# Performance work log

Measured on AMD Instinct MI355X. Metric: run time of the kernel, lower is better.

Reference implementation:

```python
import jax, jax.numpy as jnp
import numpy as np

N_EMBED = 256
N_HEADS = 4
HEAD_SIZE = N_EMBED // N_HEADS  # 64
BLOCK_SIZE = 768
LN_EPS = 1e-5


def layer_norm(x, g, b):
    mu = jnp.mean(x, axis=-1, keepdims=True)
    var = jnp.var(x, axis=-1, keepdims=True)
    return (x - mu) * jax.lax.rsqrt(var + LN_EPS) * g + b


def setup_inputs() -> dict:
    key = jax.random.key(0)
    ks = jax.random.split(key, 12)
    B, T, C, H, hs = 32, BLOCK_SIZE, N_EMBED, N_HEADS, HEAD_SIZE
    s_in = 1.0 / np.sqrt(C)
    s_ff = 1.0 / np.sqrt(4 * C)
    return {
        "x": jax.random.normal(ks[0], (B, T, C), jnp.float32),
        # per-head projections, stacked: [H, C, hs]
        "Wq": jax.random.normal(ks[1], (H, C, hs), jnp.float32) * s_in,
        "Wk": jax.random.normal(ks[2], (H, C, hs), jnp.float32) * s_in,
        "Wv": jax.random.normal(ks[3], (H, C, hs), jnp.float32) * s_in,
        "Wo": jax.random.normal(ks[4], (C, C), jnp.float32) * s_in,
        "bo": jnp.zeros((C,), jnp.float32),
        "W1": jax.random.normal(ks[5], (C, 4 * C), jnp.float32) * s_in,
        "b1": jnp.zeros((4 * C,), jnp.float32),
        "W2": jax.random.normal(ks[6], (4 * C, C), jnp.float32) * s_ff,
        "b2": jnp.zeros((C,), jnp.float32),
        "g1": jnp.ones((C,), jnp.float32),
        "be1": jnp.zeros((C,), jnp.float32),
        "g2": jnp.ones((C,), jnp.float32),
        "be2": jnp.zeros((C,), jnp.float32),
    }


def reference(x, Wq, Wk, Wv, Wo, bo, W1, b1, W2, b2, g1, be1, g2, be2):
    B, T, C = x.shape
    # --- multi-head causal self-attention (pre-LN) ---
    h = layer_norm(x, g1, be1)
    q = jnp.einsum("btc,hcd->bhtd", h, Wq)
    k = jnp.einsum("btc,hcd->bhtd", h, Wk)
    v = jnp.einsum("btc,hcd->bhtd", h, Wv)
    scores = jnp.einsum("bhtd,bhsd->bhts", q, k) * (HEAD_SIZE ** -0.5)
    causal = jnp.tril(jnp.ones((T, T), bool))
    scores = jnp.where(causal, scores, -jnp.inf)
    attn = jax.nn.softmax(scores, axis=-1)  # dropout = identity (eval)
    o = jnp.einsum("bhts,bhsd->bhtd", attn, v)
    o = o.transpose(0, 2, 1, 3).reshape(B, T, C)  # concat heads
    x = x + o @ Wo + bo
    # --- feed-forward (pre-LN) ---
    h2 = layer_norm(x, g2, be2)
    x = x + jax.nn.relu(h2 @ W1 + b1) @ W2 + b2
    return x
```

## Files before the change

### kernel.cpp

```cpp
#include <hip/hip_runtime.h>
#include <stdint.h>

using short8   = __attribute__((ext_vector_type(8))) short;
using f32x4    = __attribute__((ext_vector_type(4))) float;
using ushort4v = __attribute__((ext_vector_type(4))) unsigned short;
using uint2v   = __attribute__((ext_vector_type(2))) unsigned int;

#define CSC  0.1803368801111f
#define FIXC 20.0f

__device__ __forceinline__ unsigned short f2bf(float f) {
    unsigned int u = __builtin_bit_cast(unsigned int, f);
    u += 0x7FFFu + ((u >> 16) & 1u);
    return (unsigned short)(u >> 16);
}
__device__ __forceinline__ float bf2f(unsigned short s) {
    unsigned int u = ((unsigned int)s) << 16;
    return __builtin_bit_cast(float, u);
}
__device__ __forceinline__ unsigned pk2bf(float a, float b) {
    unsigned r;
    asm("v_cvt_pk_bf16_f32 %0, %1, %2" : "=v"(r) : "v"(a), "v"(b));
    return r;
}

__device__ __forceinline__ void gload16(const void* g, void* l) {
    __builtin_amdgcn_global_load_lds(
        (const __attribute__((address_space(1))) void*)(uintptr_t)g,
        (__attribute__((address_space(3))) void*)(unsigned)(uintptr_t)l,
        16, 0, 0);
}

__device__ __forceinline__ uint2v ln_row_pk(f32x4 v, f32x4 gv, f32x4 bvv) {
    float s  = v[0] + v[1] + v[2] + v[3];
    float s2 = v[0]*v[0] + v[1]*v[1] + v[2]*v[2] + v[3]*v[3];
    for (int m = 1; m < 64; m <<= 1) {
        s  += __shfl_xor(s,  m, 64);
        s2 += __shfl_xor(s2, m, 64);
    }
    float mu  = s * (1.0f / 256.0f);
    float var = s2 * (1.0f / 256.0f) - mu * mu;
    float rs  = rsqrtf(var + 1e-5f);
    float r0 = (v[0] - mu) * rs * gv[0] + bvv[0];
    float r1 = (v[1] - mu) * rs * gv[1] + bvv[1];
    float r2 = (v[2] - mu) * rs * gv[2] + bvv[2];
    float r3 = (v[3] - mu) * rs * gv[3] + bvv[3];
    uint2v u; u[0] = pk2bf(r0, r1); u[1] = pk2bf(r2, r3);
    return u;
}

__global__ __launch_bounds__(256) void prep_k(const float* __restrict__ x, const float* __restrict__ g1,
                                              const float* __restrict__ be1, unsigned short* __restrict__ h,
                                              const float* __restrict__ Wq, const float* __restrict__ Wk,
                                              const float* __restrict__ Wv, const float* __restrict__ Wo,
                                              const float* __restrict__ W1, const float* __restrict__ W2,
                                              unsigned short* __restrict__ wpackT, unsigned short* __restrict__ woT,
                                              unsigned short* __restrict__ w1T, unsigned short* __restrict__ w2T) {
    __shared__ float t[64][65];
    if (blockIdx.x >= 192) {
        int row  = (blockIdx.x - 192) * 4 + (threadIdx.x >> 6);
        int lane = threadIdx.x & 63;
        f32x4 v = *(const f32x4*)(x + (size_t)row * 256 + lane * 4);
        f32x4 gv = *(const f32x4*)(g1 + lane * 4);
        f32x4 bv = *(const f32x4*)(be1 + lane * 4);
        uint2v u = ln_row_pk(v, gv, bv);
        *(uint2v*)(h + (size_t)row * 256 + lane * 4) = u;
        return;
    }
    const int bid = blockIdx.x;
    const float* in; unsigned short* out;
    int R, C, r0, c0;
    if (bid < 48) {
        int z = bid >> 2, cx = bid & 3;
        int qkv = z >> 2, hh = z & 3;
        in = ((qkv == 0) ? Wq : (qkv == 1) ? Wk : Wv) + (size_t)hh * 256 * 64;
        out = wpackT + (size_t)(qkv * 256 + hh * 64) * 256;
        R = 256; C = 64; r0 = cx * 64; c0 = 0;
    } else if (bid < 64) {
        int tt = bid - 48;
        in = Wo; out = woT; R = 256; C = 256; r0 = (tt >> 2) * 64; c0 = (tt & 3) * 64;
    } else if (bid < 128) {
        int tt = bid - 64;
        in = W1; out = w1T; R = 256; C = 1024; r0 = (tt & 3) * 64; c0 = (tt >> 2) * 64;
    } else {
        int tt = bid - 128;
        in = W2; out = w2T; R = 1024; C = 256; r0 = (tt & 15) * 64; c0 = (tt >> 4) * 64;
    }
    const int tx = threadIdx.x & 63, ty = threadIdx.x >> 6;
    #pragma unroll
    for (int i = 0; i < 64; i += 4)
        t[i + ty][tx] = in[(size_t)(r0 + i + ty) * C + c0 + tx];
    __syncthreads();
    #pragma unroll
    for (int i = 0; i < 64; i += 4)
        out[(size_t)(c0 + i + ty) * R + r0 + tx] = f2bf(t[tx][i + ty]);
}

__global__ __launch_bounds__(256) void qkv_k(const unsigned short* __restrict__ h,
                                             const unsigned short* __restrict__ wpackT,
                                             unsigned short* __restrict__ qk,
                                             unsigned short* __restrict__ vT) {
    __shared__ unsigned short As[128 * 64];
    __shared__ unsigned short Bs[128 * 64];
    const int tid  = threadIdx.x;
    const int lane = tid & 63;
    const int w    = tid >> 6;
    const int wm   = w >> 1, wn = w & 1;
    const int l15  = lane & 15, l4 = lane >> 4;
    const int bid  = blockIdx.x;

    const unsigned short *A, *BT;
    unsigned short* outp;
    int bm, bn, N;
    float qsc = 1.0f;
    if (bid < 768) {
        const int xcd = bid & 7, i = bid >> 3;
        bm = xcd * 24 + (i >> 2);
        bn = i & 3;
        A = h; BT = wpackT; outp = qk; N = 512;
        if (bn < 2) qsc = CSC;
    } else {
        const int t = bid - 768;
        const int xcd = t & 7, j = t >> 3;
        bn = xcd * 24 + (j >> 1);
        bm = j & 1;
        A = wpackT + 512 * 256; BT = h; outp = vT; N = 24576;
    }
    const int K = 256;

    f32x4 acc[4][4] = {};

    const size_t K2 = (size_t)K * 2;
    const int i0   = w * 4096 + lane * 16;
    const int row0 = i0 >> 7;
    const int cb0  = (i0 & 127) ^ ((row0 & 7) << 4);
    const char* aSrc = (const char*)A  + ((size_t)(bm * 128 + row0)) * K2 + cb0;
    const char* bSrc = (const char*)BT + ((size_t)(bn * 128 + row0)) * K2 + cb0;

    for (int t = 0; t < 4; ++t) {
        {
            const char* aS = aSrc + (size_t)t * 128;
            const char* bS = bSrc + (size_t)t * 128;
            char* aD = (char*)&As[0] + w * 4096;
            char* bD = (char*)&Bs[0] + w * 4096;
            #pragma unroll
            for (int c = 0; c < 4; ++c) {
                gload16(aS + (size_t)c * 8 * K2, aD + c * 1024);
                gload16(bS + (size_t)c * 8 * K2, bD + c * 1024);
            }
        }
        __syncthreads();
        #pragma unroll
        for (int kf = 0; kf < 2; ++kf) {
            int kb = kf * 64 + l4 * 16;
            short8 af[4], bfr[4];
            #pragma unroll
            for (int mf = 0; mf < 4; ++mf) {
                int row = wm * 64 + mf * 16 + l15;
                af[mf] = *(const short8*)((const char*)&As[0] + ((row * 128 + kb) ^ ((row & 7) << 4)));
            }
            #pragma unroll
            for (int nf = 0; nf < 4; ++nf) {
                int row = wn * 64 + nf * 16 + l15;
                bfr[nf] = *(const short8*)((const char*)&Bs[0] + ((row * 128 + kb) ^ ((row & 7) << 4)));
            }
            #pragma unroll
            for (int mf = 0; mf < 4; ++mf)
                #pragma unroll
                for (int nf = 0; nf < 4; ++nf)
                    acc[mf][nf] = __builtin_amdgcn_mfma_f32_16x16x32_bf16(af[mf], bfr[nf], acc[mf][nf], 0, 0, 0);
        }
        __syncthreads();
    }

    #pragma unroll
    for (int nf = 0; nf < 4; ++nf) {
        int col = bn * 128 + wn * 64 + nf * 16 + l15;
        #pragma unroll
        for (int mf = 0; mf < 4; ++mf) {
            int row0o = bm * 128 + wm * 64 + mf * 16 + l4 * 4;
            size_t off = (size_t)row0o * N + col;
            unsigned p01 = pk2bf(acc[mf][nf][0] * qsc, acc[mf][nf][1] * qsc);
            unsigned p23 = pk2bf(acc[mf][nf][2] * qsc, acc[mf][nf][3] * qsc);
            outp[off]                 = (unsigned short)p01;
            outp[off + (size_t)N]     = (unsigned short)(p01 >> 16);
            outp[off + (size_t)N * 2] = (unsigned short)p23;
            outp[off + (size_t)N * 3] = (unsigned short)(p23 >> 16);
        }
    }
}

template <int EPI, bool DB>
__global__ __launch_bounds__(256) void gemm_bt(const unsigned short* __restrict__ A,
                                               const unsigned short* __restrict__ BT,
                                               void* __restrict__ outp,
                                               const float* __restrict__ bias,
                                               const void* __restrict__ resid,
                                               int K, int N) {
    __shared__ unsigned short As[DB ? 2 : 1][128 * 64];
    __shared__ unsigned short Bs[DB ? 2 : 1][128 * 64];
    const int tid  = threadIdx.x;
    const int lane = tid & 63;
    const int w    = tid >> 6;
    const int wm   = w >> 1, wn = w & 1;
    const int bm   = blockIdx.y, bn = blockIdx.x;
    const int l15  = lane & 15, l4 = lane >> 4;

    f32x4 acc[4][4] = {};

    const size_t K2 = (size_t)K * 2;
    const int i0   = w * 4096 + lane * 16;
    const int row0 = i0 >> 7;
    const int cb0  = (i0 & 127) ^ ((row0 & 7) << 4);
    const char* aSrc = (const char*)A  + ((size_t)(bm * 128 + row0)) * K2 + cb0;
    const char* bSrc = (const char*)BT + ((size_t)(bn * 128 + row0)) * K2 + cb0;
    const int nt = K >> 6;

    auto stage = [&](int t, int buf) {
        const char* aS = aSrc + (size_t)t * 128;
        const char* bS = bSrc + (size_t)t * 128;
        char* aD = (char*)&As[buf][0] + w * 4096;
        char* bD = (char*)&Bs[buf][0] + w * 4096;
        #pragma unroll
        for (int c = 0; c < 4; ++c) {
            gload16(aS + (size_t)c * 8 * K2, aD + c * 1024);
            gload16(bS + (size_t)c * 8 * K2, bD + c * 1024);
        }
    };
    auto compute = [&](int buf) {
        const char* AsB = (const char*)&As[buf][0];
        const char* BsB = (const char*)&Bs[buf][0];
        #pragma unroll
        for (int kf = 0; kf < 2; ++kf) {
            int kb = kf * 64 + l4 * 16;
            short8 af[4], bfr[4];
            #pragma unroll
            for (int mf = 0; mf < 4; ++mf) {
                int row = wm * 64 + mf * 16 + l15;
                af[mf] = *(const short8*)(AsB + ((row * 128 + kb) ^ ((row & 7) << 4)));
            }
            #pragma unroll
            for (int nf = 0; nf < 4; ++nf) {
                int row = wn * 64 + nf * 16 + l15;
                bfr[nf] = *(const short8*)(BsB + ((row * 128 + kb) ^ ((row & 7) << 4)));
            }
            #pragma unroll
            for (int mf = 0; mf < 4; ++mf)
                #pragma unroll
                for (int nf = 0; nf < 4; ++nf)
                    acc[mf][nf] = __builtin_amdgcn_mfma_f32_16x16x32_bf16(af[mf], bfr[nf], acc[mf][nf], 0, 0, 0);
        }
    };

    if (DB) {
        stage(0, 0);
        for (int t = 0; t < nt; ++t) {
            const int cur = t & 1;
            __syncthreads();
            if (t + 1 < nt) stage(t + 1, cur ^ 1);
            compute(cur);
        }
    } else {
        for (int t = 0; t < nt; ++t) {
            stage(t, 0);
            __syncthreads();
            compute(0);
            __syncthreads();
        }
    }

    #pragma unroll
    for (int nf = 0; nf < 4; ++nf) {
        int col = bn * 128 + wn * 64 + nf * 16 + l15;
        float bv = bias[col];
        #pragma unroll
        for (int mf = 0; mf < 4; ++mf) {
            int row0o = bm * 128 + wm * 64 + mf * 16 + l4 * 4;
            size_t off = (size_t)row0o * N + col;
            float v[4];
            #pragma unroll
            for (int r = 0; r < 4; ++r)
                v[r] = acc[mf][nf][r] + bv + ((const float*)resid)[off + (size_t)r * N];
            unsigned short* O = (unsigned short*)outp;
            unsigned p01 = pk2bf(v[0], v[1]), p23 = pk2bf(v[2], v[3]);
            O[off]                 = (unsigned short)p01;
            O[off + (size_t)N]     = (unsigned short)(p01 >> 16);
            O[off + (size_t)N * 2] = (unsigned short)p23;
            O[off + (size_t)N * 3] = (unsigned short)(p23 >> 16);
        }
    }
}

__global__ __launch_bounds__(256) void ff_fused(const unsigned short* __restrict__ x1b,
                                                const float* __restrict__ g2,
                                                const float* __restrict__ be2,
                                                const unsigned short* __restrict__ w1T,
                                                const unsigned short* __restrict__ w2T,
                                                const float* __restrict__ b1,
                                                const float* __restrict__ b2,
                                                float* __restrict__ out) {
    __shared__ unsigned short sA[4][64 * 64];
    __shared__ unsigned short sW[16384];
    __shared__ unsigned short sAct[64 * 64];
    const int tid = threadIdx.x, lane = tid & 63, w = tid >> 6;
    const int l15 = lane & 15, l4 = lane >> 4;
    const int wm = w >> 1, wn = w & 1;
    const int r0 = blockIdx.x * 64;

    {
        f32x4 gv = *(const f32x4*)(g2 + lane * 4);
        f32x4 bv = *(const f32x4*)(be2 + lane * 4);
        const int ks = lane >> 4, colb = (lane & 15) * 8;
        #pragma unroll
        for (int it = 0; it < 16; ++it) {
            int row = it * 4 + w;
            ushort4v u4 = *(const ushort4v*)(x1b + (size_t)(r0 + row) * 256 + lane * 4);
            f32x4 v;
            #pragma unroll
            for (int i = 0; i < 4; ++i) v[i] = bf2f(u4[i]);
            uint2v u = ln_row_pk(v, gv, bv);
            *(uint2v*)((char*)&sA[0][0] + ks * 8192 + row * 128 + (colb ^ ((row & 7) << 4))) = u;
        }
    }

    f32x4 oacc[2][8] = {};

    for (int c = 0; c < 16; ++c) {
        {
            const char* wb = (const char*)w1T + (size_t)(c * 64) * 512;
            #pragma unroll
            for (int g = 0; g < 8; ++g) {
                int j = g * 4096 + tid * 16;
                int ks = j >> 13, row = (j >> 7) & 63, cb = j & 127;
                gload16(wb + (size_t)row * 512 + ks * 128 + (cb ^ ((row & 7) << 4)),
                        (char*)&sW[0] + j);
            }
        }
        __syncthreads();

        f32x4 aacc[2][2] = {};
        __builtin_amdgcn_s_setprio(1);
        #pragma unroll
        for (int ks = 0; ks < 4; ++ks) {
            #pragma unroll
            for (int kf = 0; kf < 2; ++kf) {
                const int kb = kf * 64 + l4 * 16;
                short8 hf[2], wf[2];
                #pragma unroll
                for (int mf = 0; mf < 2; ++mf) {
                    int row = wm * 32 + mf * 16 + l15;
                    hf[mf] = *(const short8*)((const char*)&sA[ks][0] + ((row * 128 + kb) ^ ((row & 7) << 4)));
                }
                #pragma unroll
                for (int nf = 0; nf < 2; ++nf) {
                    int row = wn * 32 + nf * 16 + l15;
                    wf[nf] = *(const short8*)((const char*)&sW[ks * 4096] + ((row * 128 + kb) ^ ((row & 7) << 4)));
                }
                #pragma unroll
                for (int mf = 0; mf < 2; ++mf)
                    #pragma unroll
                    for (int nf = 0; nf < 2; ++nf)
                        aacc[mf][nf] = __builtin_amdgcn_mfma_f32_16x16x32_bf16(wf[nf], hf[mf], aacc[mf][nf], 0, 0, 0);
            }
        }
        __builtin_amdgcn_s_setprio(0);
        #pragma unroll
        for (int mf = 0; mf < 2; ++mf)
            #pragma unroll
            for (int nf = 0; nf < 2; ++nf) {
                int nl = wn * 32 + nf * 16 + l4 * 4;
                f32x4 bv = *(const f32x4*)(b1 + c * 64 + nl);
                float v0 = aacc[mf][nf][0] + bv[0]; v0 = v0 > 0.0f ? v0 : 0.0f;
                float v1 = aacc[mf][nf][1] + bv[1]; v1 = v1 > 0.0f ? v1 : 0.0f;
                float v2 = aacc[mf][nf][2] + bv[2]; v2 = v2 > 0.0f ? v2 : 0.0f;
                float v3 = aacc[mf][nf][3] + bv[3]; v3 = v3 > 0.0f ? v3 : 0.0f;
                uint2v u; u[0] = pk2bf(v0, v1); u[1] = pk2bf(v2, v3);
                int m = wm * 32 + mf * 16 + l15;
                *(uint2v*)((char*)&sAct[0] + ((m * 128 + nl * 2) ^ ((m & 7) << 4))) = u;
            }
        __syncthreads();

        {
            const char* wb = (const char*)w2T + (size_t)c * 128;
            #pragma unroll
            for (int g = 0; g < 8; ++g) {
                int j = g * 4096 + tid * 16;
                int row = j >> 7, cb = j & 127;
                gload16(wb + (size_t)row * 2048 + (cb ^ ((row & 7) << 4)),
                        (char*)&sW[0] + j);
            }
        }
        __syncthreads();

        __builtin_amdgcn_s_setprio(1);
        #pragma unroll
        for (int kf = 0; kf < 2; ++kf) {
            const int kb = kf * 64 + l4 * 16;
            short8 af[2], wf[8];
            #pragma unroll
            for (int mf = 0; mf < 2; ++mf) {
                int row = wm * 32 + mf * 16 + l15;
                af[mf] = *(const short8*)((const char*)&sAct[0] + ((row * 128 + kb) ^ ((row & 7) << 4)));
            }
            #pragma unroll
            for (int nf = 0; nf < 8; ++nf) {
                int row = wn * 128 + nf * 16 + l15;
                wf[nf] = *(const short8*)((const char*)&sW[0] + ((row * 128 + kb) ^ ((row & 7) << 4)));
            }
            #pragma unroll
            for (int mf = 0; mf < 2; ++mf)
                #pragma unroll
                for (int nf = 0; nf < 8; ++nf)
                    oacc[mf][nf] = __builtin_amdgcn_mfma_f32_16x16x32_bf16(af[mf], wf[nf], oacc[mf][nf], 0, 0, 0);
        }
        __builtin_amdgcn_s_setprio(0);
        __syncthreads();
    }

    #pragma unroll
    for (int nf = 0; nf < 8; ++nf) {
        const int col = wn * 128 + nf * 16 + l15;
        const float bv = b2[col];
        #pragma unroll
        for (int mf = 0; mf < 2; ++mf) {
            const int row = r0 + wm * 32 + mf * 16 + l4 * 4;
            const size_t off = (size_t)row * 256 + col;
            #pragma unroll
            for (int r = 0; r < 4; ++r)
                out[off + (size_t)r * 256] = oacc[mf][nf][r] + bv + bf2f(x1b[off + (size_t)r * 256]);
        }
    }
}

__global__ __launch_bounds__(256) void attn_k(const unsigned short* __restrict__ qk,
                                              const unsigned short* __restrict__ vT,
                                              unsigned short* __restrict__ o) {
    __shared__ unsigned short Ks[2][64 * 64];
    __shared__ unsigned short Vt[2][64 * 64];
    __shared__ unsigned short Pl[4][16 * 64];
    const int tid = threadIdx.x, lane = tid & 63, w = tid >> 6;
    const int l15 = lane & 15, l4 = lane >> 4;
    const int gid = blockIdx.x;
    const int xcd = gid & 7, slot = gid >> 3;
    const int sl6 = slot / 6;
    const int bh  = xcd * 16 + sl6;
    const int x   = slot - sl6 * 6;
    const int qb1 = x, qb2 = 11 - x;
    const int b = bh >> 2, h = bh & 3;
    const unsigned short* Qb = qk + (size_t)b * 768 * 512 + h * 64;
    const char* Kg = (const char*)(Qb + 256);
    const char* Vg = (const char*)(vT + (size_t)(h * 64) * 24576 + (size_t)b * 768);
    const int t01 = qb1 * 64, t02 = qb2 * 64;
    const int tq1 = t01 + w * 16 + l15;
    const int tq2 = t02 + w * 16 + l15;

    short8 q1f0 = *(const short8*)(Qb + (size_t)tq1 * 512 + l4 * 8);
    short8 q1f1 = *(const short8*)(Qb + (size_t)tq1 * 512 + 32 + l4 * 8);
    short8 q2f0 = *(const short8*)(Qb + (size_t)tq2 * 512 + l4 * 8);
    short8 q2f1 = *(const short8*)(Qb + (size_t)tq2 * 512 + 32 + l4 * 8);

    const int srow = w * 16 + (lane >> 3);
    const int scb  = ((lane & 7) * 16) ^ ((srow & 7) << 4);
    const char* kSrc = Kg + (size_t)srow * 1024 + scb;
    const char* vSrc = Vg + (size_t)srow * 49152 + scb;
    char* kDst0 = (char*)&Ks[0][0] + w * 2048;
    char* vDst0 = (char*)&Vt[0][0] + w * 2048;

    f32x4 oA[4] = {}, oB[4] = {};
    float lsA = 0.0f, lsB = 0.0f;
    unsigned short* Pw = &Pl[w][0];
    const char* KsB;
    const char* VtB;
    int sb = 0;

    auto do_tile = [&](short8 qf0, short8 qf1, f32x4 (&oacc)[4], float& lsum, bool diag, int tq) {
        f32x4 sacc[4] = {};
        __builtin_amdgcn_s_setprio(1);
        #pragma unroll
        for (int kf = 0; kf < 2; ++kf) {
            const int kb = kf * 64 + l4 * 16;
            short8 qf = kf ? qf1 : qf0;
            #pragma unroll
            for (int nf = 0; nf < 4; ++nf) {
                int sr = nf * 16 + l15;
                short8 kfr = *(const short8*)(KsB + ((sr * 128 + kb) ^ ((sr & 7) << 4)));
                sacc[nf] = __builtin_amdgcn_mfma_f32_16x16x32_bf16(kfr, qf, sacc[nf], 0, 0, 0);
            }
        }
        __builtin_amdgcn_s_setprio(0);

        if (diag) {
            #pragma unroll
            for (int nf = 0; nf < 4; ++nf)
                #pragma unroll
                for (int r = 0; r < 4; ++r) {
                    int s = sb * 64 + nf * 16 + l4 * 4 + r;
                    if (s > tq) sacc[nf][r] = -1e30f;
                }
        }
        float psum = 0.0f;
        #pragma unroll
        for (int nf = 0; nf < 4; ++nf) {
            float p0 = __builtin_amdgcn_exp2f(sacc[nf][0] - FIXC);
            float p1 = __builtin_amdgcn_exp2f(sacc[nf][1] - FIXC);
            float p2 = __builtin_amdgcn_exp2f(sacc[nf][2] - FIXC);
            float p3 = __builtin_amdgcn_exp2f(sacc[nf][3] - FIXC);
            psum += (p0 + p1) + (p2 + p3);
            uint2v u; u[0] = pk2bf(p0, p1); u[1] = pk2bf(p2, p3);
            *(uint2v*)((char*)Pw + ((l15 * 128 + nf * 32 + l4 * 8) ^ ((l15 & 7) << 4))) = u;
        }
        psum += __shfl_xor(psum, 16, 64);
        psum += __shfl_xor(psum, 32, 64);
        lsum += psum;

        __builtin_amdgcn_s_setprio(1);
        #pragma unroll
        for (int kf = 0; kf < 2; ++kf) {
            const int kb = kf * 64 + l4 * 16;
            short8 pa = *(const short8*)((const char*)Pw + ((l15 * 128 + kb) ^ ((l15 & 7) << 4)));
            #pragma unroll
            for (int nf = 0; nf < 4; ++nf) {
                int dr = nf * 16 + l15;
                short8 vfr = *(const short8*)(VtB + ((dr * 128 + kb) ^ ((dr & 7) << 4)));
                oacc[nf] = __builtin_amdgcn_mfma_f32_16x16x32_bf16(pa, vfr, oacc[nf], 0, 0, 0);
            }
        }
        __builtin_amdgcn_s_setprio(0);
    };

    gload16(kSrc, kDst0);                 gload16(kSrc + 8 * 1024, kDst0 + 1024);
    gload16(vSrc, vDst0);                 gload16(vSrc + 8 * 49152, vDst0 + 1024);

    for (sb = 0; sb <= qb2; ++sb) {
        const int pb = sb & 1;
        __syncthreads();
        if (sb < qb2) {
            const char* ks = kSrc + (size_t)(sb + 1) * 65536;
            const char* vs = vSrc + (size_t)(sb + 1) * 128;
            char* kd = kDst0 + (pb ^ 1) * 8192;
            char* vd = vDst0 + (pb ^ 1) * 8192;
            gload16(ks, kd);              gload16(ks + 8 * 1024, kd + 1024);
            gload16(vs, vd);              gload16(vs + 8 * 49152, vd + 1024);
        }
        KsB = (const char*)&Ks[0][0] + pb * 8192;
        VtB = (const char*)&Vt[0][0] + pb * 8192;

        do_tile(q2f0, q2f1, oB, lsB, sb == qb2, tq2);
        if (sb <= qb1) do_tile(q1f0, q1f1, oA, lsA, sb == qb1, tq1);
    }

    float liA = 1.0f / lsA, liB = 1.0f / lsB;
    float lrA[4], lrB[4];
    #pragma unroll
    for (int r = 0; r < 4; ++r) {
        lrA[r] = __shfl(liA, l4 * 4 + r, 64);
        lrB[r] = __shfl(liB, l4 * 4 + r, 64);
    }
    const int tA = t01 + w * 16 + l4 * 4;
    const int tB = t02 + w * 16 + l4 * 4;
    unsigned short* oa = o + ((size_t)(b * 768 + tA)) * 256 + h * 64;
    unsigned short* ob = o + ((size_t)(b * 768 + tB)) * 256 + h * 64;
    #pragma unroll
    for (int nf = 0; nf < 4; ++nf) {
        unsigned a01 = pk2bf(oA[nf][0] * lrA[0], oA[nf][1] * lrA[1]);
        unsigned a23 = pk2bf(oA[nf][2] * lrA[2], oA[nf][3] * lrA[3]);
        unsigned b01 = pk2bf(oB[nf][0] * lrB[0], oB[nf][1] * lrB[1]);
        unsigned b23 = pk2bf(oB[nf][2] * lrB[2], oB[nf][3] * lrB[3]);
        oa[nf * 16 + l15]       = (unsigned short)a01;
        oa[256 + nf * 16 + l15] = (unsigned short)(a01 >> 16);
        oa[512 + nf * 16 + l15] = (unsigned short)a23;
        oa[768 + nf * 16 + l15] = (unsigned short)(a23 >> 16);
        ob[nf * 16 + l15]       = (unsigned short)b01;
        ob[256 + nf * 16 + l15] = (unsigned short)(b01 >> 16);
        ob[512 + nf * 16 + l15] = (unsigned short)b23;
        ob[768 + nf * 16 + l15] = (unsigned short)(b23 >> 16);
    }
}

extern "C" void kernel_launch(void* const* d_in, const int* in_sizes, int n_in,
                              void* d_out, int out_size, void* d_ws, size_t ws_size,
                              hipStream_t stream) {
    const float* x   = (const float*)d_in[0];
    const float* Wq  = (const float*)d_in[1];
    const float* Wk  = (const float*)d_in[2];
    const float* Wv  = (const float*)d_in[3];
    const float* Wo  = (const float*)d_in[4];
    const float* bo  = (const float*)d_in[5];
    const float* W1  = (const float*)d_in[6];
    const float* b1  = (const float*)d_in[7];
    const float* W2  = (const float*)d_in[8];
    const float* b2  = (const float*)d_in[9];
    const float* g1  = (const float*)d_in[10];
    const float* be1 = (const float*)d_in[11];
    const float* g2  = (const float*)d_in[12];
    const float* be2 = (const float*)d_in[13];

    char* ws = (char*)d_ws;
    unsigned short* qk_ws  = (unsigned short*)(ws + 0);
    unsigned short* vT_ws  = (unsigned short*)(ws + 25165824);
    unsigned short* o_ws   = (unsigned short*)(ws + 37748736);
    unsigned short* h_ws   = (unsigned short*)(ws + 50331648);
    unsigned short* x1b_ws = (unsigned short*)(ws + 62914560);
    unsigned short* wpackT = (unsigned short*)(ws + 88080384);
    unsigned short* woT    = (unsigned short*)(ws + 88473600);
    unsigned short* w1T    = (unsigned short*)(ws + 88604672);
    unsigned short* w2T    = (unsigned short*)(ws + 89128960);

    prep_k<<<6336, 256, 0, stream>>>(x, g1, be1, h_ws, Wq, Wk, Wv, Wo, W1, W2, wpackT, woT, w1T, w2T);
    qkv_k<<<1152, 256, 0, stream>>>(h_ws, wpackT, qk_ws, vT_ws);
    attn_k<<<768, 256, 0, stream>>>(qk_ws, vT_ws, o_ws);
    gemm_bt<2, true><<<dim3(2, 192), 256, 0, stream>>>(o_ws, woT, x1b_ws, bo, x, 256, 256);
    ff_fused<<<384, 256, 0, stream>>>(x1b_ws, g2, be2, w1T, w2T, b1, b2, (float*)d_out);
}
```

Before: 117.4 us.

## Enlarge FF row tile to 96 and double-buffer W1/W2 staging in fused FFN

```diff
diff --git a/kernel.cpp b/kernel.cpp
--- a/kernel.cpp
+++ b/kernel.cpp
@@ -299,65 +299,82 @@
                                                 const float* __restrict__ b1,
                                                 const float* __restrict__ b2,
                                                 float* __restrict__ out) {
-    __shared__ unsigned short sA[4][64 * 64];
-    __shared__ unsigned short sW[16384];
-    __shared__ unsigned short sAct[64 * 64];
+    __shared__ unsigned short sA[4][96 * 64];
+    __shared__ unsigned short sW1[16384];
+    __shared__ unsigned short sW2[16384];
+    __shared__ unsigned short sAct[96 * 64];
     const int tid = threadIdx.x, lane = tid & 63, w = tid >> 6;
     const int l15 = lane & 15, l4 = lane >> 4;
     const int wm = w >> 1, wn = w & 1;
-    const int r0 = blockIdx.x * 64;
+    const int r0 = blockIdx.x * 96;
 
     {
         f32x4 gv = *(const f32x4*)(g2 + lane * 4);
         f32x4 bv = *(const f32x4*)(be2 + lane * 4);
         const int ks = lane >> 4, colb = (lane & 15) * 8;
         #pragma unroll
-        for (int it = 0; it < 16; ++it) {
+        for (int it = 0; it < 24; ++it) {
             int row = it * 4 + w;
             ushort4v u4 = *(const ushort4v*)(x1b + (size_t)(r0 + row) * 256 + lane * 4);
             f32x4 v;
             #pragma unroll
-            for (int i = 0; i < 4; ++i) v[i] = bf2f(u4[i]);
+            for (int q = 0; q < 4; ++q) v[q] = bf2f(u4[q]);
             uint2v u = ln_row_pk(v, gv, bv);
-            *(uint2v*)((char*)&sA[0][0] + ks * 8192 + row * 128 + (colb ^ ((row & 7) << 4))) = u;
-        }
-    }
-
-    f32x4 oacc[2][8] = {};
+            *(uint2v*)((char*)&sA[0][0] + ks * 12288 + row * 128 + (colb ^ ((row & 7) << 4))) = u;
+        }
+    }
+
+    auto stage_w1 = [&](int c) {
+        const char* wb = (const char*)w1T + (size_t)(c * 64) * 512;
+        #pragma unroll
+        for (int g = 0; g < 8; ++g) {
+            int j = g * 4096 + tid * 16;
+            int ks = j >> 13, row = (j >> 7) & 63, cb = j & 127;
+            gload16(wb + (size_t)row * 512 + ks * 128 + (cb ^ ((row & 7) << 4)),
+                    (char*)&sW1[0] + j);
+        }
+    };
+    auto stage_w2 = [&](int c) {
+        const char* wb = (const char*)w2T + (size_t)c * 128;
+        #pragma unroll
+        for (int g = 0; g < 8; ++g) {
+            int j = g * 4096 + tid * 16;
+            int row = j >> 7, cb = j & 127;
+            gload16(wb + (size_t)row * 2048 + (cb ^ ((row & 7) << 4)),
+                    (char*)&sW2[0] + j);
+        }
+    };
+
+    stage_w1(0);
+    __syncthreads();
+
+    f32x4 oacc[3][8] = {};
 
     for (int c = 0; c < 16; ++c) {
-        {
-            const char* wb = (const char*)w1T + (size_t)(c * 64) * 512;
-            #pragma unroll
-            for (int g = 0; g < 8; ++g) {
-                int j = g * 4096 + tid * 16;
-                int ks = j >> 13, row = (j >> 7) & 63, cb = j & 127;
-                gload16(wb + (size_t)row * 512 + ks * 128 + (cb ^ ((row & 7) << 4)),
-                        (char*)&sW[0] + j);
-            }
-        }
-        __syncthreads();
-
-        f32x4 aacc[2][2] = {};
+        stage_w2(c);
+
+        f32x4 aacc[3][2] = {};
         __builtin_amdgcn_s_setprio(1);
         #pragma unroll
         for (int ks = 0; ks < 4; ++ks) {
             #pragma unroll
             for (int kf = 0; kf < 2; ++kf) {
                 const int kb = kf * 64 + l4 * 16;
-                short8 hf[2], wf[2];
+                short8 hf[3], wf[2];
                 #pragma unroll
-                for (int mf = 0; mf < 2; ++mf) {
-                    int row = wm * 32 + mf * 16 + l15;
-                    hf[mf] = *(const short8*)((const char*)&sA[ks][0] + ((row * 128 + kb) ^ ((row & 7) << 4)));
+                for (int mf = 0; mf < 3; ++mf) {
+                    int row = wm * 48 + mf * 16 + l15;
+                    hf[mf] = *(const short8*)((const char*)&sA[0][0] + ks * 12288
+                               + ((row * 128 + kb) ^ ((row & 7) << 4)));
                 }
                 #pragma unroll
                 for (int nf = 0; nf < 2; ++nf) {
                     int row = wn * 32 + nf * 16 + l15;
-                    wf[nf] = *(const short8*)((const char*)&sW[ks * 4096] + ((row * 128 + kb) ^ ((row & 7) << 4)));
+                    wf[nf] = *(const short8*)((const char*)&sW1[0] + ks * 8192
+                               + ((row * 128 + kb) ^ ((row & 7) << 4)));
                 }
                 #pragma unroll
-                for (int mf = 0; mf < 2; ++mf)
+                for (int mf = 0; mf < 3; ++mf)
                     #pragma unroll
                     for (int nf = 0; nf < 2; ++nf)
                         aacc[mf][nf] = __builtin_amdgcn_mfma_f32_16x16x32_bf16(wf[nf], hf[mf], aacc[mf][nf], 0, 0, 0);
@@ -365,7 +382,7 @@
         }
         __builtin_amdgcn_s_setprio(0);
         #pragma unroll
-        for (int mf = 0; mf < 2; ++mf)
+        for (int mf = 0; mf < 3; ++mf)
             #pragma unroll
             for (int nf = 0; nf < 2; ++nf) {
                 int nl = wn * 32 + nf * 16 + l4 * 4;
@@ -375,45 +392,37 @@
                 float v2 = aacc[mf][nf][2] + bv[2]; v2 = v2 > 0.0f ? v2 : 0.0f;
                 float v3 = aacc[mf][nf][3] + bv[3]; v3 = v3 > 0.0f ? v3 : 0.0f;
                 uint2v u; u[0] = pk2bf(v0, v1); u[1] = pk2bf(v2, v3);
-                int m = wm * 32 + mf * 16 + l15;
+                int m = wm * 48 + mf * 16 + l15;
                 *(uint2v*)((char*)&sAct[0] + ((m * 128 + nl * 2) ^ ((m & 7) << 4))) = u;
             }
+
         __syncthreads();
 
-        {
-            const char* wb = (const char*)w2T + (size_t)c * 128;
-            #pragma unroll
-            for (int g = 0; g < 8; ++g) {
-                int j = g * 4096 + tid * 16;
-                int row = j >> 7, cb = j & 127;
-                gload16(wb + (size_t)row * 2048 + (cb ^ ((row & 7) << 4)),
-                        (char*)&sW[0] + j);
-            }
-        }
-        __syncthreads();
+        if (c + 1 < 16) stage_w1(c + 1);
 
         __builtin_amdgcn_s_setprio(1);
         #pragma unroll
         for (int kf = 0; kf < 2; ++kf) {
             const int kb = kf * 64 + l4 * 16;
-            short8 af[2], wf[8];
-            #pragma unroll
-            for (int mf = 0; mf < 2; ++mf) {
-                int row = wm * 32 + mf * 16 + l15;
-                af[mf] = *(const short8*)((const char*)&sAct[0] + ((row * 128 + kb) ^ ((row & 7) << 4)));
+            short8 af[3], wf[8];
+            #pragma unroll
+            for (int mf = 0; mf < 3; ++mf) {
+                int m = wm * 48 + mf * 16 + l15;
+                af[mf] = *(const short8*)((const char*)&sAct[0] + ((m * 128 + kb) ^ ((m & 7) << 4)));
             }
             #pragma unroll
             for (int nf = 0; nf < 8; ++nf) {
-                int row = wn * 128 + nf * 16 + l15;
-                wf[nf] = *(const short8*)((const char*)&sW[0] + ((row * 128 + kb) ^ ((row & 7) << 4)));
-            }
-            #pragma unroll
-            for (int mf = 0; mf < 2; ++mf)
+                int n2 = wn * 128 + nf * 16 + l15;
+                wf[nf] = *(const short8*)((const char*)&sW2[0] + ((n2 * 128 + kb) ^ ((n2 & 7) << 4)));
+            }
+            #pragma unroll
+            for (int mf = 0; mf < 3; ++mf)
                 #pragma unroll
                 for (int nf = 0; nf < 8; ++nf)
                     oacc[mf][nf] = __builtin_amdgcn_mfma_f32_16x16x32_bf16(af[mf], wf[nf], oacc[mf][nf], 0, 0, 0);
         }
         __builtin_amdgcn_s_setprio(0);
+
         __syncthreads();
     }
 
@@ -422,8 +431,8 @@
         const int col = wn * 128 + nf * 16 + l15;
         const float bv = b2[col];
         #pragma unroll
-        for (int mf = 0; mf < 2; ++mf) {
-            const int row = r0 + wm * 32 + mf * 16 + l4 * 4;
+        for (int mf = 0; mf < 3; ++mf) {
+            const int row = r0 + wm * 48 + mf * 16 + l4 * 4;
             const size_t off = (size_t)row * 256 + col;
             #pragma unroll
             for (int r = 0; r < 4; ++r)
@@ -610,5 +619,5 @@
     qkv_k<<<1152, 256, 0, stream>>>(h_ws, wpackT, qk_ws, vT_ws);
     attn_k<<<768, 256, 0, stream>>>(qk_ws, vT_ws, o_ws);
     gemm_bt<2, true><<<dim3(2, 192), 256, 0, stream>>>(o_ws, woT, x1b_ws, bo, x, 256, 256);
-    ff_fused<<<384, 256, 0, stream>>>(x1b_ws, g2, be2, w1T, w2T, b1, b2, (float*)d_out);
-}
+    ff_fused<<<256, 256, 0, stream>>>(x1b_ws, g2, be2, w1T, w2T, b1, b2, (float*)d_out);
+}
```

Result: no change. 115.1 us (-2.0%).
